# Kernel tuning notes

Hardware: AMD Instinct MI355X
Metric: run time of the kernel (lower is better)

## Reference

```python
import jax, jax.numpy as jnp
import numpy as np

H = 16  # num_attention_heads


def setup_inputs() -> dict:
    key = jax.random.key(0)
    ks = jax.random.split(key, 4)
    B, S, D = 2, 2048, 1024
    hidden_states = jax.random.normal(ks[0], (B, S, D), dtype=jnp.float32)
    attention_mask = jnp.zeros((B, 1, 1, S), dtype=jnp.float32)
    scale = 1.0 / np.sqrt(D)
    Wq = jax.random.normal(ks[1], (D, D), dtype=jnp.float32) * scale
    Wk = jax.random.normal(ks[2], (D, D), dtype=jnp.float32) * scale
    Wv = jax.random.normal(ks[3], (D, D), dtype=jnp.float32) * scale
    bq = jnp.zeros((D,), dtype=jnp.float32)
    bk = jnp.zeros((D,), dtype=jnp.float32)
    bv = jnp.zeros((D,), dtype=jnp.float32)
    return {"hidden_states": hidden_states, "attention_mask": attention_mask,
            "Wq": Wq, "bq": bq, "Wk": Wk, "bk": bk, "Wv": Wv, "bv": bv}


def reference(hidden_states, attention_mask, Wq, bq, Wk, bk, Wv, bv):
    B, S, D = hidden_states.shape
    Dh = D // H

    def proj(W, b):
        # torch Linear: x @ W.T + b ; reshape to [B, H, S, Dh]
        y = jnp.einsum('bsd,ed->bse', hidden_states, W) + b
        return y.reshape(B, S, H, Dh).transpose(0, 2, 1, 3)

    q = proj(Wq, bq)
    k = proj(Wk, bk)
    v = proj(Wv, bv)

    scores = jnp.einsum('bhqd,bhkd->bhqk', q, k) / jnp.sqrt(jnp.float32(Dh))
    scores = scores + attention_mask  # additive mask broadcast [B,1,1,S]
    probs = jax.nn.softmax(scores, axis=-1)  # [B,H,Sq,Sk]
    out_attention_scores = probs.sum(axis=-2).sum(axis=-2)  # [B, Sk]
    # dropout prob = 0 (eval) -> identity
    context = jnp.einsum('bhqk,bhkd->bhqd', probs, v)
    context = context.transpose(0, 2, 1, 3).reshape(B, S, D)
    return context, out_attention_scores
```

## Files before the change

### kernel.cpp

```cpp
#include <hip/hip_runtime.h>
#include <hip/hip_bf16.h>
#include <stdint.h>

typedef unsigned short u16;
typedef __attribute__((ext_vector_type(8))) unsigned short u16x8;
typedef __attribute__((ext_vector_type(4))) unsigned short u16x4;
typedef __attribute__((ext_vector_type(8))) __bf16 bf16x8;
typedef __attribute__((ext_vector_type(4))) float f32x4;

#define LOG2E 1.44269504088896340736f

#if defined(__has_builtin)
#if __has_builtin(__builtin_amdgcn_exp2f)
#define EXP2(x) __builtin_amdgcn_exp2f(x)
#endif
#endif
#ifndef EXP2
#define EXP2(x) exp2f(x)
#endif

__device__ __forceinline__ f32x4 mfma16(u16x8 a, u16x8 b, f32x4 c) {
  return __builtin_amdgcn_mfma_f32_16x16x32_bf16(
      __builtin_bit_cast(bf16x8, a), __builtin_bit_cast(bf16x8, b), c, 0, 0, 0);
}

__device__ __forceinline__ u16 f2bf(float f) {
  unsigned u = __builtin_bit_cast(unsigned, f);
  return (u16)((u + 0x7fffu + ((u >> 16) & 1u)) >> 16);
}

__device__ __forceinline__ unsigned cvtpk(float a, float b) {
  unsigned r;
  asm volatile("v_cvt_pk_bf16_f32 %0, %1, %2" : "=v"(r) : "v"(a), "v"(b));
  return r;
}

__device__ __forceinline__ void gload_lds16(const void* g, void* l) {
  __builtin_amdgcn_global_load_lds(
      (__attribute__((address_space(1))) void*)const_cast<void*>(g),
      (__attribute__((address_space(3))) void*)l, 16, 0, 0);
}

#define SWZ(row, colbyte) ((((row) * 128) + (colbyte)) ^ (((row) & 7) << 4))

__global__ void cast_f32_bf16(const float* __restrict__ src, u16* __restrict__ dst, int n4) {
  int i = blockIdx.x * blockDim.x + threadIdx.x;
  if (i < n4) {
    f32x4 v = ((const f32x4*)src)[i];
    u16x4 o;
    o[0] = f2bf(v[0]); o[1] = f2bf(v[1]); o[2] = f2bf(v[2]); o[3] = f2bf(v[3]);
    ((u16x4*)dst)[i] = o;
  }
}

__global__ void cast3_f32_bf16(const float* __restrict__ s0, const float* __restrict__ s1,
                               const float* __restrict__ s2, u16* __restrict__ dst) {
  const int seg = blockIdx.x >> 10;
  const int i = (blockIdx.x & 1023) * blockDim.x + threadIdx.x;
  const float* src = (seg == 0) ? s0 : ((seg == 1) ? s1 : s2);
  f32x4 v = ((const f32x4*)src)[i];
  u16x4 o;
  o[0] = f2bf(v[0]); o[1] = f2bf(v[1]); o[2] = f2bf(v[2]); o[3] = f2bf(v[3]);
  ((u16x4*)(dst + (size_t)seg * 1048576))[i] = o;
}

__global__ __launch_bounds__(256) void gemm_qkv(
    const u16* __restrict__ A, const u16* __restrict__ Bm,
    const float* __restrict__ bq, const float* __restrict__ bk, const float* __restrict__ bv,
    u16* __restrict__ Qb, u16* __restrict__ Kb, u16* __restrict__ VTb) {
  __shared__ __align__(16) u16 Asm[128 * 32];
  __shared__ __align__(16) u16 Bsm[128 * 32];
  const int tid = threadIdx.x;
  const int wave = tid >> 6, lane = tid & 63;
  const int lq = lane & 15, lg = lane >> 4;
  const int wr = wave >> 1, wc = wave & 1;
  const int m0 = blockIdx.y * 128, n0 = blockIdx.x * 128;

  f32x4 zero = {0.f, 0.f, 0.f, 0.f};
  f32x4 acc[4][4];
#pragma unroll
  for (int mi = 0; mi < 4; ++mi)
#pragma unroll
    for (int ni = 0; ni < 4; ++ni) acc[mi][ni] = zero;

  for (int kt = 0; kt < 32; ++kt) {
    const int k0 = kt * 32;
    __syncthreads();
#pragma unroll
    for (int c = 0; c < 2; ++c) {
      const int idx = wave * 2 + c;
      const u16* ga = A + (size_t)(m0 + idx * 16 + (lane >> 2)) * 1024 + k0 + (lane & 3) * 8;
      gload_lds16(ga, (char*)Asm + idx * 1024);
      const u16* gb = Bm + (size_t)(n0 + idx * 16 + (lane >> 2)) * 1024 + k0 + (lane & 3) * 8;
      gload_lds16(gb, (char*)Bsm + idx * 1024);
    }
    __syncthreads();

    u16x8 af[4], bfr[4];
#pragma unroll
    for (int mi = 0; mi < 4; ++mi)
      af[mi] = *(const u16x8*)&Asm[(wr * 64 + mi * 16 + lq) * 32 + lg * 8];
#pragma unroll
    for (int ni = 0; ni < 4; ++ni)
      bfr[ni] = *(const u16x8*)&Bsm[(wc * 64 + ni * 16 + lq) * 32 + lg * 8];
#pragma unroll
    for (int mi = 0; mi < 4; ++mi)
#pragma unroll
      for (int ni = 0; ni < 4; ++ni)
        acc[mi][ni] = mfma16(af[mi], bfr[ni], acc[mi][ni]);
  }

  const int which = n0 >> 10;
  const float* bias = (which == 0) ? bq : ((which == 1) ? bk : bv);
  const float scl = (which == 0) ? (0.125f * LOG2E) : 1.0f;
#pragma unroll
  for (int mi = 0; mi < 4; ++mi) {
    const int m = m0 + wr * 64 + mi * 16 + lg * 4;
    const int bb = m >> 11;
    const int s = m & 2047;
#pragma unroll
    for (int ni = 0; ni < 4; ++ni) {
      const int n = n0 + wc * 64 + ni * 16 + lq;
      const int d = n & 1023;
      const int h = d >> 6, dh = d & 63;
      const float bi = bias[d];
#pragma unroll
      for (int r = 0; r < 4; ++r) {
        float v = (acc[mi][ni][r] + bi) * scl;
        if (which == 2)
          VTb[(((size_t)bb * 16 + h) * 64 + dh) * 2048 + (size_t)(s + r)] = f2bf(v);
        else {
          u16* dst = (which == 0) ? Qb : Kb;
          dst[(((size_t)bb * 16 + h) * 2048 + (size_t)(s + r)) * 64 + dh] = f2bf(v);
        }
      }
    }
  }
}

__global__ __launch_bounds__(512) void attn_main(
    const u16* __restrict__ Qb, const u16* __restrict__ Kb, const u16* __restrict__ VTb,
    const float* __restrict__ maskg, float* __restrict__ out_ctx, float* __restrict__ winv) {
  __shared__ __align__(16) u16 Kl[2][4096];
  __shared__ __align__(16) u16 VTl[2][4096];
  __shared__ __align__(16) u16 Pl[8][1024];

  const int tid = threadIdx.x;
  const int w = tid >> 6, lane = tid & 63;
  const int lq = lane & 15, lg = lane >> 4;
  const int bid = (blockIdx.x & 7) * 64 + (blockIdx.x >> 3);
  const int qt = bid & 15, bh = bid >> 4;
  const int b = bh >> 4, h = bh & 15;
  const int qw = qt * 128 + w * 16;

  const u16* qp = Qb + ((size_t)bh * 2048 + qw + lq) * 64 + lg * 8;
  const u16x8 qa0 = *(const u16x8*)qp;
  const u16x8 qa1 = *(const u16x8*)(qp + 32);

  const char* Kbase = (const char*)(Kb + (size_t)bh * 2048 * 64);
  const char* VTbase = (const char*)(VTb + (size_t)bh * 64 * 2048);
  const float* mbase = maskg + b * 2048;

  const int srow = tid >> 3;
  const int scol = ((tid & 7) * 16) ^ ((srow & 7) << 4);
  char* kd0 = (char*)&Kl[0][0] + w * 1024;
  char* kd1 = (char*)&Kl[1][0] + w * 1024;
  char* vd0 = (char*)&VTl[0][0] + w * 1024;
  char* vd1 = (char*)&VTl[1][0] + w * 1024;

  auto stageK = [&](int kt, int buf) {
    gload_lds16(Kbase + (size_t)(kt * 64 + srow) * 128 + scol, buf ? kd1 : kd0);
  };
  auto stageVT = [&](int kt, int buf) {
    gload_lds16(VTbase + (size_t)srow * 4096 + (size_t)kt * 128 + scol, buf ? vd1 : vd0);
  };

  f32x4 acc[4];
  {
    f32x4 zero = {0.f, 0.f, 0.f, 0.f};
#pragma unroll
    for (int ni = 0; ni < 4; ++ni) acc[ni] = zero;
  }
  float l_l = 0.f;
  char* Pw = (char*)&Pl[w][0];

  stageK(0, 0);
  stageVT(0, 0);
  __syncthreads();
  for (int kt = 0; kt < 32; ++kt) {
    const int cur = kt & 1;
    if (kt + 1 < 32) { stageK(kt + 1, cur ^ 1); stageVT(kt + 1, cur ^ 1); }
    const char* Kt = (const char*)&Kl[cur][0];
    const char* Vt = (const char*)&VTl[cur][0];

#pragma unroll
    for (int chunk = 0; chunk < 4; ++chunk) {
      const int krow = chunk * 16 + lq;
      const u16x8 ka0 = *(const u16x8*)(Kt + SWZ(krow, lg * 16));
      const u16x8 ka1 = *(const u16x8*)(Kt + SWZ(krow, 64 + lg * 16));
      f32x4 z = {0.f, 0.f, 0.f, 0.f};
      f32x4 s = mfma16(ka0, qa0, z);
      s = mfma16(ka1, qa1, s);
      const f32x4 mv = *(const f32x4*)(mbase + kt * 64 + chunk * 16 + lg * 4);
      float p[4];
#pragma unroll
      for (int r = 0; r < 4; ++r) {
        p[r] = EXP2(fmaf(mv[r], LOG2E, s[r]));
        l_l += p[r];
      }
      uint2 wp;
      wp.x = cvtpk(p[0], p[1]); wp.y = cvtpk(p[2], p[3]);
      *(uint2*)(Pw + SWZ(lq, chunk * 32 + lg * 8)) = wp;
    }

#pragma unroll
    for (int kc = 0; kc < 2; ++kc) {
      const u16x8 pa = *(const u16x8*)(Pw + SWZ(lq, kc * 64 + lg * 16));
#pragma unroll
      for (int ni = 0; ni < 4; ++ni) {
        const u16x8 vb = *(const u16x8*)(Vt + SWZ(ni * 16 + lq, kc * 64 + lg * 16));
        acc[ni] = mfma16(pa, vb, acc[ni]);
      }
    }
    __syncthreads();
  }

  l_l += __shfl_xor(l_l, 16);
  l_l += __shfl_xor(l_l, 32);
  const float il = 1.0f / l_l;
  if (lg == 0) winv[bh * 2048 + qw + lq] = il;

  f32x4 il4;
#pragma unroll
  for (int r = 0; r < 4; ++r) il4[r] = __shfl(il, lg * 4 + r);

  const int qrow = b * 2048 + qw + lg * 4;
#pragma unroll
  for (int ni = 0; ni < 4; ++ni) {
    const int dh = h * 64 + ni * 16 + lq;
#pragma unroll
    for (int r = 0; r < 4; ++r)
      out_ctx[(size_t)(qrow + r) * 1024 + dh] = acc[ni][r] * il4[r];
  }
}

__global__ __launch_bounds__(256) void colsum_kernel(
    const u16* __restrict__ Qb, const u16* __restrict__ Kb,
    const float* __restrict__ maskg, const float* __restrict__ winv,
    float* __restrict__ out_cs) {
  __shared__ __align__(16) u16 Ql[2][4096];

  const int tid = threadIdx.x;
  const int w = tid >> 6, lane = tid & 63;
  const int lq = lane & 15, lg = lane >> 4;
  const int bid = (blockIdx.x & 7) * 128 + (blockIdx.x >> 3);
  const int ktile = bid & 31, bh = bid >> 5;
  const int b = bh >> 4;
  const int kbase = ktile * 64 + w * 16;

  const u16* kp = Kb + ((size_t)bh * 2048 + kbase + lq) * 64 + lg * 8;
  const u16x8 kb0 = *(const u16x8*)kp, kb1 = *(const u16x8*)(kp + 32);
  const float mvl = maskg[b * 2048 + kbase + lq] * LOG2E;
  const float* wbase = winv + bh * 2048;
  const char* Qbase = (const char*)(Qb + (size_t)bh * 2048 * 64);

  const int r0 = tid >> 3;
  const int scol = ((tid & 7) * 16) ^ ((r0 & 7) << 4);
  char* qd0 = (char*)&Ql[0][0] + w * 1024;
  char* qd1 = (char*)&Ql[1][0] + w * 1024;
  auto stageQ = [&](int qt, int buf) {
    const char* src = Qbase + (size_t)(qt * 64) * 128;
    char* d = buf ? qd1 : qd0;
    gload_lds16(src + (size_t)r0 * 128 + scol, d);
    gload_lds16(src + (size_t)(r0 + 32) * 128 + scol, d + 4096);
  };

  float c = 0.f;
  stageQ(0, 0);
  __syncthreads();
  for (int qt = 0; qt < 32; ++qt) {
    const int cur = qt & 1;
    if (qt + 1 < 32) stageQ(qt + 1, cur ^ 1);
    const char* Qt = (const char*)&Ql[cur][0];
#pragma unroll
    for (int chunk = 0; chunk < 4; ++chunk) {
      const u16x8 qf0 = *(const u16x8*)(Qt + SWZ(chunk * 16 + lq, lg * 16));
      const u16x8 qf1 = *(const u16x8*)(Qt + SWZ(chunk * 16 + lq, 64 + lg * 16));
      f32x4 z = {0.f, 0.f, 0.f, 0.f};
      f32x4 s = mfma16(qf0, kb0, z);
      s = mfma16(qf1, kb1, s);
      const f32x4 wv = *(const f32x4*)(wbase + qt * 64 + chunk * 16 + lg * 4);
      c += EXP2(s[0] + mvl) * wv[0] + EXP2(s[1] + mvl) * wv[1] +
           EXP2(s[2] + mvl) * wv[2] + EXP2(s[3] + mvl) * wv[3];
    }
    __syncthreads();
  }
  c += __shfl_xor(c, 16);
  c += __shfl_xor(c, 32);
  if (lg == 0) atomicAdd(&out_cs[b * 2048 + kbase + lq], c);
}

extern "C" void kernel_launch(void* const* d_in, const int* in_sizes, int n_in,
                              void* d_out, int out_size, void* d_ws, size_t ws_size,
                              hipStream_t stream) {
  (void)in_sizes; (void)n_in; (void)out_size; (void)ws_size;
  const float* X    = (const float*)d_in[0];
  const float* mask = (const float*)d_in[1];
  const float* Wq   = (const float*)d_in[2];
  const float* bq   = (const float*)d_in[3];
  const float* Wk   = (const float*)d_in[4];
  const float* bk   = (const float*)d_in[5];
  const float* Wv   = (const float*)d_in[6];
  const float* bv   = (const float*)d_in[7];
  float* out = (float*)d_out;

  char* ws = (char*)d_ws;
  u16* Xb   = (u16*)(ws);
  u16* Wcat = (u16*)(ws + 8388608);
  u16* Qb   = (u16*)(ws + 14680064);
  u16* Kb   = (u16*)(ws + 23068672);
  u16* VTb  = (u16*)(ws + 31457280);
  float* winv = (float*)(ws + 39845888);

  cast_f32_bf16<<<4096, 256, 0, stream>>>(X, Xb, 1048576);
  cast3_f32_bf16<<<3072, 256, 0, stream>>>(Wq, Wk, Wv, Wcat);

  hipMemsetAsync(out + 4194304, 0, 4096 * sizeof(float), stream);

  gemm_qkv<<<dim3(24, 32), 256, 0, stream>>>(Xb, Wcat, bq, bk, bv, Qb, Kb, VTb);

  attn_main<<<512, 512, 0, stream>>>(Qb, Kb, VTb, mask, out, winv);
  colsum_kernel<<<1024, 256, 0, stream>>>(Qb, Kb, mask, winv, out + 4194304);
}
```

Measured before the change: 158.8 us.

## Triple-buffer LDS staging with vmcnt waits across GEMM, attention and colsum kernels

```diff
diff --git a/kernel.cpp b/kernel.cpp
--- a/kernel.cpp
+++ b/kernel.cpp
@@ -39,6 +39,11 @@
   __builtin_amdgcn_global_load_lds(
       (__attribute__((address_space(1))) void*)const_cast<void*>(g),
       (__attribute__((address_space(3))) void*)l, 16, 0, 0);
+}
+
+template<int N> __device__ __forceinline__ void vmwait() {
+  asm volatile("s_waitcnt vmcnt(%0)" :: "n"(N) : "memory");
+  __builtin_amdgcn_sched_barrier(0);
 }
 
 #define SWZ(row, colbyte) ((((row) * 128) + (colbyte)) ^ (((row) & 7) << 4))
@@ -68,13 +73,15 @@
     const u16* __restrict__ A, const u16* __restrict__ Bm,
     const float* __restrict__ bq, const float* __restrict__ bk, const float* __restrict__ bv,
     u16* __restrict__ Qb, u16* __restrict__ Kb, u16* __restrict__ VTb) {
-  __shared__ __align__(16) u16 Asm[128 * 32];
-  __shared__ __align__(16) u16 Bsm[128 * 32];
+  __shared__ __align__(16) u16 Asm[3][4096];
+  __shared__ __align__(16) u16 Bsm[3][4096];
   const int tid = threadIdx.x;
   const int wave = tid >> 6, lane = tid & 63;
   const int lq = lane & 15, lg = lane >> 4;
   const int wr = wave >> 1, wc = wave & 1;
-  const int m0 = blockIdx.y * 128, n0 = blockIdx.x * 128;
+  const int lin = blockIdx.y * 24 + blockIdx.x;
+  const int wg = (lin & 7) * 96 + (lin >> 3);
+  const int m0 = (wg / 24) * 128, n0 = (wg % 24) * 128;
 
   f32x4 zero = {0.f, 0.f, 0.f, 0.f};
   f32x4 acc[4][4];
@@ -83,31 +90,40 @@
 #pragma unroll
     for (int ni = 0; ni < 4; ++ni) acc[mi][ni] = zero;
 
-  for (int kt = 0; kt < 32; ++kt) {
+  auto stage = [&](int kt, int buf) {
     const int k0 = kt * 32;
-    __syncthreads();
 #pragma unroll
     for (int c = 0; c < 2; ++c) {
       const int idx = wave * 2 + c;
       const u16* ga = A + (size_t)(m0 + idx * 16 + (lane >> 2)) * 1024 + k0 + (lane & 3) * 8;
-      gload_lds16(ga, (char*)Asm + idx * 1024);
+      gload_lds16(ga, (char*)&Asm[buf][0] + idx * 1024);
       const u16* gb = Bm + (size_t)(n0 + idx * 16 + (lane >> 2)) * 1024 + k0 + (lane & 3) * 8;
-      gload_lds16(gb, (char*)Bsm + idx * 1024);
-    }
-    __syncthreads();
-
+      gload_lds16(gb, (char*)&Bsm[buf][0] + idx * 1024);
+    }
+  };
+
+  stage(0, 0);
+  stage(1, 1);
+  for (int kt = 0; kt < 32; ++kt) {
+    if (kt < 31) vmwait<4>(); else vmwait<0>();
+    __builtin_amdgcn_s_barrier();
+    if (kt + 2 < 32) stage(kt + 2, (kt + 2) % 3);
+    const int cur = kt % 3;
+
+    __builtin_amdgcn_s_setprio(1);
     u16x8 af[4], bfr[4];
 #pragma unroll
     for (int mi = 0; mi < 4; ++mi)
-      af[mi] = *(const u16x8*)&Asm[(wr * 64 + mi * 16 + lq) * 32 + lg * 8];
+      af[mi] = *(const u16x8*)&Asm[cur][(wr * 64 + mi * 16 + lq) * 32 + lg * 8];
 #pragma unroll
     for (int ni = 0; ni < 4; ++ni)
-      bfr[ni] = *(const u16x8*)&Bsm[(wc * 64 + ni * 16 + lq) * 32 + lg * 8];
+      bfr[ni] = *(const u16x8*)&Bsm[cur][(wc * 64 + ni * 16 + lq) * 32 + lg * 8];
 #pragma unroll
     for (int mi = 0; mi < 4; ++mi)
 #pragma unroll
       for (int ni = 0; ni < 4; ++ni)
         acc[mi][ni] = mfma16(af[mi], bfr[ni], acc[mi][ni]);
+    __builtin_amdgcn_s_setprio(0);
   }
 
   const int which = n0 >> 10;
@@ -141,8 +157,8 @@
 __global__ __launch_bounds__(512) void attn_main(
     const u16* __restrict__ Qb, const u16* __restrict__ Kb, const u16* __restrict__ VTb,
     const float* __restrict__ maskg, float* __restrict__ out_ctx, float* __restrict__ winv) {
-  __shared__ __align__(16) u16 Kl[2][4096];
-  __shared__ __align__(16) u16 VTl[2][4096];
+  __shared__ __align__(16) u16 Kl[3][4096];
+  __shared__ __align__(16) u16 VTl[3][4096];
   __shared__ __align__(16) u16 Pl[8][1024];
 
   const int tid = threadIdx.x;
@@ -163,16 +179,12 @@
 
   const int srow = tid >> 3;
   const int scol = ((tid & 7) * 16) ^ ((srow & 7) << 4);
-  char* kd0 = (char*)&Kl[0][0] + w * 1024;
-  char* kd1 = (char*)&Kl[1][0] + w * 1024;
-  char* vd0 = (char*)&VTl[0][0] + w * 1024;
-  char* vd1 = (char*)&VTl[1][0] + w * 1024;
 
   auto stageK = [&](int kt, int buf) {
-    gload_lds16(Kbase + (size_t)(kt * 64 + srow) * 128 + scol, buf ? kd1 : kd0);
+    gload_lds16(Kbase + (size_t)(kt * 64 + srow) * 128 + scol, (char*)&Kl[buf][0] + w * 1024);
   };
   auto stageVT = [&](int kt, int buf) {
-    gload_lds16(VTbase + (size_t)srow * 4096 + (size_t)kt * 128 + scol, buf ? vd1 : vd0);
+    gload_lds16(VTbase + (size_t)srow * 4096 + (size_t)kt * 128 + scol, (char*)&VTl[buf][0] + w * 1024);
   };
 
   f32x4 acc[4];
@@ -184,15 +196,21 @@
   float l_l = 0.f;
   char* Pw = (char*)&Pl[w][0];
 
-  stageK(0, 0);
-  stageVT(0, 0);
-  __syncthreads();
+  stageK(0, 0); stageVT(0, 0);
+  stageK(1, 1); stageVT(1, 1);
   for (int kt = 0; kt < 32; ++kt) {
-    const int cur = kt & 1;
-    if (kt + 1 < 32) { stageK(kt + 1, cur ^ 1); stageVT(kt + 1, cur ^ 1); }
+    if (kt < 31) vmwait<2>(); else vmwait<0>();
+    __builtin_amdgcn_s_barrier();
+    if (kt + 2 < 32) {
+      const int nb = (kt + 2) % 3;
+      stageK(kt + 2, nb);
+      stageVT(kt + 2, nb);
+    }
+    const int cur = kt % 3;
     const char* Kt = (const char*)&Kl[cur][0];
     const char* Vt = (const char*)&VTl[cur][0];
 
+    __builtin_amdgcn_s_setprio(1);
 #pragma unroll
     for (int chunk = 0; chunk < 4; ++chunk) {
       const int krow = chunk * 16 + lq;
@@ -222,7 +240,7 @@
         acc[ni] = mfma16(pa, vb, acc[ni]);
       }
     }
-    __syncthreads();
+    __builtin_amdgcn_s_setprio(0);
   }
 
   l_l += __shfl_xor(l_l, 16);
@@ -248,56 +266,65 @@
     const u16* __restrict__ Qb, const u16* __restrict__ Kb,
     const float* __restrict__ maskg, const float* __restrict__ winv,
     float* __restrict__ out_cs) {
-  __shared__ __align__(16) u16 Ql[2][4096];
+  __shared__ __align__(16) u16 Ql[3][4096];
 
   const int tid = threadIdx.x;
   const int w = tid >> 6, lane = tid & 63;
   const int lq = lane & 15, lg = lane >> 4;
-  const int bid = (blockIdx.x & 7) * 128 + (blockIdx.x >> 3);
-  const int ktile = bid & 31, bh = bid >> 5;
+  const int bid = (blockIdx.x & 7) * 64 + (blockIdx.x >> 3);
+  const int ktile = bid & 15, bh = bid >> 4;
   const int b = bh >> 4;
-  const int kbase = ktile * 64 + w * 16;
-
-  const u16* kp = Kb + ((size_t)bh * 2048 + kbase + lq) * 64 + lg * 8;
-  const u16x8 kb0 = *(const u16x8*)kp, kb1 = *(const u16x8*)(kp + 32);
-  const float mvl = maskg[b * 2048 + kbase + lq] * LOG2E;
+  const int kbase = ktile * 128 + w * 32;
+
+  const u16* kp0 = Kb + ((size_t)bh * 2048 + kbase + lq) * 64 + lg * 8;
+  const u16* kp1 = kp0 + 16 * 64;
+  const u16x8 kb00 = *(const u16x8*)kp0, kb01 = *(const u16x8*)(kp0 + 32);
+  const u16x8 kb10 = *(const u16x8*)kp1, kb11 = *(const u16x8*)(kp1 + 32);
+  const float mvl0 = maskg[b * 2048 + kbase + lq] * LOG2E;
+  const float mvl1 = maskg[b * 2048 + kbase + 16 + lq] * LOG2E;
   const float* wbase = winv + bh * 2048;
   const char* Qbase = (const char*)(Qb + (size_t)bh * 2048 * 64);
 
   const int r0 = tid >> 3;
   const int scol = ((tid & 7) * 16) ^ ((r0 & 7) << 4);
-  char* qd0 = (char*)&Ql[0][0] + w * 1024;
-  char* qd1 = (char*)&Ql[1][0] + w * 1024;
   auto stageQ = [&](int qt, int buf) {
     const char* src = Qbase + (size_t)(qt * 64) * 128;
-    char* d = buf ? qd1 : qd0;
+    char* d = (char*)&Ql[buf][0] + w * 1024;
     gload_lds16(src + (size_t)r0 * 128 + scol, d);
     gload_lds16(src + (size_t)(r0 + 32) * 128 + scol, d + 4096);
   };
 
-  float c = 0.f;
+  float c0 = 0.f, c1 = 0.f;
   stageQ(0, 0);
-  __syncthreads();
+  stageQ(1, 1);
   for (int qt = 0; qt < 32; ++qt) {
-    const int cur = qt & 1;
-    if (qt + 1 < 32) stageQ(qt + 1, cur ^ 1);
-    const char* Qt = (const char*)&Ql[cur][0];
+    if (qt < 31) vmwait<2>(); else vmwait<0>();
+    __builtin_amdgcn_s_barrier();
+    if (qt + 2 < 32) stageQ(qt + 2, (qt + 2) % 3);
+    const char* Qt = (const char*)&Ql[qt % 3][0];
 #pragma unroll
     for (int chunk = 0; chunk < 4; ++chunk) {
       const u16x8 qf0 = *(const u16x8*)(Qt + SWZ(chunk * 16 + lq, lg * 16));
       const u16x8 qf1 = *(const u16x8*)(Qt + SWZ(chunk * 16 + lq, 64 + lg * 16));
       f32x4 z = {0.f, 0.f, 0.f, 0.f};
-      f32x4 s = mfma16(qf0, kb0, z);
-      s = mfma16(qf1, kb1, s);
+      f32x4 s0 = mfma16(qf0, kb00, z);
+      s0 = mfma16(qf1, kb01, s0);
+      f32x4 s1 = mfma16(qf0, kb10, z);
+      s1 = mfma16(qf1, kb11, s1);
       const f32x4 wv = *(const f32x4*)(wbase + qt * 64 + chunk * 16 + lg * 4);
-      c += EXP2(s[0] + mvl) * wv[0] + EXP2(s[1] + mvl) * wv[1] +
-           EXP2(s[2] + mvl) * wv[2] + EXP2(s[3] + mvl) * wv[3];
-    }
-    __syncthreads();
-  }
-  c += __shfl_xor(c, 16);
-  c += __shfl_xor(c, 32);
-  if (lg == 0) atomicAdd(&out_cs[b * 2048 + kbase + lq], c);
+#pragma unroll
+      for (int r = 0; r < 4; ++r) {
+        c0 += EXP2(s0[r] + mvl0) * wv[r];
+        c1 += EXP2(s1[r] + mvl1) * wv[r];
+      }
+    }
+  }
+  c0 += __shfl_xor(c0, 16); c0 += __shfl_xor(c0, 32);
+  c1 += __shfl_xor(c1, 16); c1 += __shfl_xor(c1, 32);
+  if (lg == 0) {
+    atomicAdd(&out_cs[b * 2048 + kbase + lq], c0);
+    atomicAdd(&out_cs[b * 2048 + kbase + 16 + lq], c1);
+  }
 }
 
 extern "C" void kernel_launch(void* const* d_in, const int* in_sizes, int n_in,
@@ -330,5 +357,5 @@
   gemm_qkv<<<dim3(24, 32), 256, 0, stream>>>(Xb, Wcat, bq, bk, bv, Qb, Kb, VTb);
 
   attn_main<<<512, 512, 0, stream>>>(Qb, Kb, VTb, mask, out, winv);
-  colsum_kernel<<<1024, 256, 0, stream>>>(Qb, Kb, mask, winv, out + 4194304);
-}
+  colsum_kernel<<<512, 256, 0, stream>>>(Qb, Kb, mask, winv, out + 4194304);
+}
```

After: 142.1 us. 10.5% less time.
